# Performance work log

Hardware: AMD Instinct MI355X
Metric: run time of the kernel (lower is better)

Reference implementation:

```python
import jax, jax.numpy as jnp
import numpy as np
import math

B, T, C, H, E = 1, 384, 512, 8, 16
D = C // H

def layer_norm(x, w, b, eps=1e-5):
    mu = jnp.mean(x, axis=-1, keepdims=True)
    var = jnp.mean(jnp.square(x - mu), axis=-1, keepdims=True)
    return (x - mu) * jax.lax.rsqrt(var + eps) * w + b

def setup_inputs() -> dict:
    key = jax.random.key(0)
    ks = jax.random.split(key, 12)
    s = 0.02
    return {
        'x': jax.random.normal(ks[0], (B, T, C), jnp.float32),
        'bias_matrix': jax.random.randint(ks[1], (B, T, T), 0, E, jnp.int32),
        'ln1_w': jnp.ones((C,), jnp.float32),
        'ln1_b': jnp.zeros((C,), jnp.float32),
        'w_attn_w': jax.random.normal(ks[2], (3 * C, C), jnp.float32) * s,
        'w_attn_b': jnp.zeros((3 * C,), jnp.float32),
        'w_proj_w': jax.random.normal(ks[3], (C, C), jnp.float32) * s,
        'w_proj_b': jnp.zeros((C,), jnp.float32),
        'attn_bias_emb': jax.random.normal(ks[4], (E, H), jnp.float32) * s,
        'edge_emb': jax.random.normal(ks[5], (E, C), jnp.float32) * s,
        'w_edge_k_w': jax.random.normal(ks[6], (C, C), jnp.float32) * s,
        'w_edge_k_b': jnp.zeros((C,), jnp.float32),
        'w_edge_v_w': jax.random.normal(ks[7], (C, C), jnp.float32) * s,
        'w_edge_v_b': jnp.zeros((C,), jnp.float32),
        'ln2_w': jnp.ones((C,), jnp.float32),
        'ln2_b': jnp.zeros((C,), jnp.float32),
        'c_fc_w': jax.random.normal(ks[8], (4 * C, C), jnp.float32) * s,
        'c_fc_b': jnp.zeros((4 * C,), jnp.float32),
        'c_proj_w': jax.random.normal(ks[9], (C, 4 * C), jnp.float32) * s,
        'c_proj_b': jnp.zeros((C,), jnp.float32),
    }

def reference(x, bias_matrix, ln1_w, ln1_b, w_attn_w, w_attn_b, w_proj_w, w_proj_b,
              attn_bias_emb, edge_emb, w_edge_k_w, w_edge_k_b, w_edge_v_w, w_edge_v_b,
              ln2_w, ln2_b, c_fc_w, c_fc_b, c_proj_w, c_proj_b):
    # --- attention branch ---
    h = layer_norm(x, ln1_w, ln1_b)
    qkv = h @ w_attn_w.T + w_attn_b                      # (B,T,3C)
    q, k, v = jnp.split(qkv, 3, axis=-1)
    q = q.reshape(B, T, H, D).transpose(0, 2, 1, 3)      # (B,H,T,D)
    k = k.reshape(B, T, H, D).transpose(0, 2, 1, 3)
    v = v.reshape(B, T, H, D).transpose(0, 2, 1, 3)
    scale = math.sqrt(D)

    ee = edge_emb[bias_matrix]                           # (B,T,T,C)
    e_k = (ee @ w_edge_k_w.T + w_edge_k_b).reshape(B, T, T, H, D)
    # score[b,h,i,j] = sum_d q[b,h,i,d] * k[b,h,j,d] * e_k[b,i,j,h,d]
    scores = jnp.einsum('bhid,bhjd,bijhd->bhij', q, k, e_k) / scale

    mask = jnp.tril(jnp.ones((T, T), bool))              # causal, diag included
    scores = jnp.where(mask, scores, -jnp.inf)
    ab = attn_bias_emb[bias_matrix].transpose(0, 3, 1, 2)  # (B,H,T,T)
    ab = jnp.where(mask, ab, 0.0)
    attn = jax.nn.softmax(scores + ab, axis=-1)

    e_v = (ee @ w_edge_v_w.T + w_edge_v_b).reshape(B, T, T, H, D)
    # y[b,h,i,d] = sum_j attn[b,h,i,j] * v[b,h,j,d] * e_v[b,i,j,h,d]
    y = jnp.einsum('bhij,bhjd,bijhd->bhid', attn, v, e_v)
    y = y.transpose(0, 2, 1, 3).reshape(B, T, C)
    y = y @ w_proj_w.T + w_proj_b
    x = x + y

    # --- MLP branch ---
    h2 = layer_norm(x, ln2_w, ln2_b)
    h2 = jax.nn.gelu(h2 @ c_fc_w.T + c_fc_b, approximate=False)
    x = x + (h2 @ c_proj_w.T + c_proj_b)
    return x
```

## Files before the change

### kernel.cpp

```cpp
#include <hip/hip_runtime.h>
#include <math.h>

#define TT 384
#define CC 512
#define HH 8
#define EE 16

typedef __bf16 bf16_t;
typedef __bf16 bf16x8 __attribute__((ext_vector_type(8)));
typedef __bf16 bf16x4v __attribute__((ext_vector_type(4)));
typedef float f32x4 __attribute__((ext_vector_type(4)));

__device__ __forceinline__ float wave_reduce_sum(float v) {
#pragma unroll
  for (int off = 32; off >= 1; off >>= 1) v += __shfl_xor(v, off, 64);
  return v;
}
__device__ __forceinline__ float wave_reduce_max(float v) {
#pragma unroll
  for (int off = 32; off >= 1; off >>= 1) v = fmaxf(v, __shfl_xor(v, off, 64));
  return v;
}

struct PreArgs {
  const float *x, *ln1w, *ln1b, *wattn, *wattnb, *eemb, *wekw, *wekb, *wevw,
      *wevb, *ln2w, *ln2b, *cfcw, *cfcb, *wproj, *wcproj;
  float *ektab, *evtab, *xmu, *xrs, *x1s1, *x1s2, *s1q, *cq, *s1f, *cf;
  bf16_t *wqkv_bf, *wfc_bf, *wproj_bf, *wcproj_bf;
};

__device__ __forceinline__ void wrow_unit(const float* __restrict__ wr,
                                          const float* __restrict__ g,
                                          const float* __restrict__ bb,
                                          float extra_c, bf16_t* __restrict__ orow,
                                          float* __restrict__ s1p,
                                          float* __restrict__ cp, int lane) {
  const float* p = wr + lane * 8;
  f32x4 w0 = *(const f32x4*)p, w1 = *(const f32x4*)(p + 4);
  f32x4 g0 = *(const f32x4*)(g + lane * 8), g1 = *(const f32x4*)(g + lane * 8 + 4);
  f32x4 b0 = *(const f32x4*)(bb + lane * 8), b1 = *(const f32x4*)(bb + lane * 8 + 4);
  f32x4 p0 = w0 * g0, p1 = w1 * g1;
  bf16x8 o;
  o[0] = (bf16_t)p0.x; o[1] = (bf16_t)p0.y; o[2] = (bf16_t)p0.z; o[3] = (bf16_t)p0.w;
  o[4] = (bf16_t)p1.x; o[5] = (bf16_t)p1.y; o[6] = (bf16_t)p1.z; o[7] = (bf16_t)p1.w;
  *(bf16x8*)(orow + lane * 8) = o;
  float s1 = p0.x + p0.y + p0.z + p0.w + p1.x + p1.y + p1.z + p1.w;
  float c = w0.x * b0.x + w0.y * b0.y + w0.z * b0.z + w0.w * b0.w +
            w1.x * b1.x + w1.y * b1.y + w1.z * b1.z + w1.w * b1.w;
  s1 = wave_reduce_sum(s1);
  c = wave_reduce_sum(c);
  if (lane == 0) { *s1p = s1; *cp = c + extra_c; }
}

__global__ __launch_bounds__(256) void pre_k(PreArgs P) {
  int b = blockIdx.x, tid = threadIdx.x, lane = tid & 63, wave = tid >> 6;
  if (b < 256) {
    int wid = b * 4 + wave;
    int gbase = wid * 16;
    int table = gbase >> 13;
    int e = (gbase >> 9) & 15;
    int c0 = gbase & 511;
    const float* er = P.eemb + e * 512 + lane * 8;
    f32x4 ea = *(const f32x4*)er;
    f32x4 eb = *(const f32x4*)(er + 4);
    const float* wbase = table ? P.wevw : P.wekw;
    const float* bbase = table ? P.wevb : P.wekb;
    float* obase = (table ? P.evtab : P.ektab) + e * 512;
#pragma unroll
    for (int o = 0; o < 16; o++) {
      int c = c0 + o;
      const float* wr = wbase + (size_t)c * 512 + lane * 8;
      f32x4 wa = *(const f32x4*)wr;
      f32x4 wb = *(const f32x4*)(wr + 4);
      float acc = ea.x * wa.x + ea.y * wa.y + ea.z * wa.z + ea.w * wa.w +
                  eb.x * wb.x + eb.y * wb.y + eb.z * wb.z + eb.w * wb.w;
      acc = wave_reduce_sum(acc);
      if (lane == 0) obase[c] = acc + bbase[c];
    }
  } else if (b < 640) {
    int n = (b - 256) * 4 + wave;
    wrow_unit(P.wattn + (size_t)n * 512, P.ln1w, P.ln1b, P.wattnb[n],
              P.wqkv_bf + (size_t)n * 512, P.s1q + n, P.cq + n, lane);
  } else if (b < 1152) {
    int n = (b - 640) * 4 + wave;
    wrow_unit(P.cfcw + (size_t)n * 512, P.ln2w, P.ln2b, P.cfcb[n],
              P.wfc_bf + (size_t)n * 512, P.s1f + n, P.cf + n, lane);
  } else if (b < 1216) {
    int base = (b - 1152) * 1024;
    for (int u = tid; u < 1024; u += 256) {
      f32x4 a = *((const f32x4*)P.wproj + base + u);
      bf16x4v o;
      o[0] = (bf16_t)a.x; o[1] = (bf16_t)a.y; o[2] = (bf16_t)a.z; o[3] = (bf16_t)a.w;
      *((bf16x4v*)P.wproj_bf + base + u) = o;
    }
  } else if (b < 1472) {
    int base = (b - 1216) * 1024;
    for (int u = tid; u < 1024; u += 256) {
      f32x4 a = *((const f32x4*)P.wcproj + base + u);
      bf16x4v o;
      o[0] = (bf16_t)a.x; o[1] = (bf16_t)a.y; o[2] = (bf16_t)a.z; o[3] = (bf16_t)a.w;
      *((bf16x4v*)P.wcproj_bf + base + u) = o;
    }
  } else if (b < 1568) {
    int r = (b - 1472) * 4 + wave;
    const float* xr = P.x + (size_t)r * 512 + lane * 8;
    f32x4 a = *(const f32x4*)xr, c = *(const f32x4*)(xr + 4);
    float s = a.x + a.y + a.z + a.w + c.x + c.y + c.z + c.w;
    float q = a.x * a.x + a.y * a.y + a.z * a.z + a.w * a.w +
              c.x * c.x + c.y * c.y + c.z * c.z + c.w * c.w;
    s = wave_reduce_sum(s);
    q = wave_reduce_sum(q);
    if (lane == 0) {
      float mu = s * (1.0f / 512.0f);
      float var = q * (1.0f / 512.0f) - mu * mu;
      P.xmu[r] = mu;
      P.xrs[r] = rsqrtf(var + 1e-5f);
    }
  } else {
    for (int i = tid; i < 384; i += 256) { P.x1s1[i] = 0.f; P.x1s2[i] = 0.f; }
  }
}

template <int MODE>
__global__ __launch_bounds__(256) void gemm_k(
    const void* __restrict__ Aptr, const bf16_t* __restrict__ Wb,
    const float* __restrict__ e0, const float* __restrict__ e1,
    const float* __restrict__ e2, const float* __restrict__ e3,
    const float* __restrict__ res, void* __restrict__ out,
    float* __restrict__ st1, float* __restrict__ st2, int N, int K) {
  constexpr bool AF32 = (MODE == 0 || MODE == 2);
  __shared__ float part[4][32][32];
  int tid = threadIdx.x, lane = tid & 63, wave = tid >> 6;
  int m0 = blockIdx.y * 32, n0 = blockIdx.x * 32;
  int r16 = lane & 15, quad = lane >> 4;
  int kchunk = K >> 2, k0 = wave * kchunk;

  f32x4 acc[2][2];
  f32x4 zero = {0.f, 0.f, 0.f, 0.f};
#pragma unroll
  for (int i = 0; i < 2; i++)
#pragma unroll
    for (int j = 0; j < 2; j++) acc[i][j] = zero;

  const float* Af = (const float*)Aptr + (size_t)(m0 + r16) * K + k0 + quad * 8;
  const bf16_t* Ab = (const bf16_t*)Aptr + (size_t)(m0 + r16) * K + k0 + quad * 8;
  const bf16_t* Wp = Wb + (size_t)(n0 + r16) * K + k0 + quad * 8;
  for (int kb = 0; kb < kchunk; kb += 32) {
    bf16x8 af[2], bfr[2];
#pragma unroll
    for (int t = 0; t < 2; t++) {
      if (AF32) {
        f32x4 a = *(const f32x4*)(Af + (size_t)t * 16 * K + kb);
        f32x4 c = *(const f32x4*)(Af + (size_t)t * 16 * K + kb + 4);
        af[t][0] = (bf16_t)a.x; af[t][1] = (bf16_t)a.y;
        af[t][2] = (bf16_t)a.z; af[t][3] = (bf16_t)a.w;
        af[t][4] = (bf16_t)c.x; af[t][5] = (bf16_t)c.y;
        af[t][6] = (bf16_t)c.z; af[t][7] = (bf16_t)c.w;
      } else {
        af[t] = *(const bf16x8*)(Ab + (size_t)t * 16 * K + kb);
      }
    }
#pragma unroll
    for (int t = 0; t < 2; t++)
      bfr[t] = *(const bf16x8*)(Wp + (size_t)t * 16 * K + kb);
#pragma unroll
    for (int i = 0; i < 2; i++)
#pragma unroll
      for (int j = 0; j < 2; j++)
        acc[i][j] = __builtin_amdgcn_mfma_f32_16x16x32_bf16(af[i], bfr[j],
                                                            acc[i][j], 0, 0, 0);
  }

#pragma unroll
  for (int i = 0; i < 2; i++)
#pragma unroll
    for (int j = 0; j < 2; j++)
#pragma unroll
      for (int r = 0; r < 4; r++)
        part[wave][i * 16 + quad * 4 + r][j * 16 + r16] = acc[i][j][r];
  __syncthreads();

  int row = tid >> 3, c4 = (tid & 7) * 4;
  f32x4 v = *(const f32x4*)&part[0][row][c4];
  v += *(const f32x4*)&part[1][row][c4];
  v += *(const f32x4*)&part[2][row][c4];
  v += *(const f32x4*)&part[3][row][c4];
  int grow = m0 + row, gcol = n0 + c4;

  if (MODE == 0 || MODE == 2) {
    float mu, rs;
    if (MODE == 0) {
      mu = e0[grow]; rs = e1[grow];
    } else {
      float S = e0[grow], Q = e1[grow];
      mu = S * (1.0f / 512.0f);
      float var = Q * (1.0f / 512.0f) - mu * mu;
      rs = rsqrtf(var + 1e-5f);
    }
    f32x4 s1v = *(const f32x4*)(e2 + gcol);
    f32x4 ccv = *(const f32x4*)(e3 + gcol);
#pragma unroll
    for (int t = 0; t < 4; t++) {
      float x = rs * (v[t] - mu * s1v[t]) + ccv[t];
      if (MODE == 2) x = 0.5f * x * (1.0f + erff(x * 0.70710678118654752f));
      v[t] = x;
    }
    bf16x4v o;
#pragma unroll
    for (int t = 0; t < 4; t++) o[t] = (bf16_t)v[t];
    *(bf16x4v*)((bf16_t*)out + (size_t)grow * N + gcol) = o;
  } else {
    v += *(const f32x4*)(e2 + gcol);
    v += *(const f32x4*)(res + (size_t)grow * N + gcol);
    *(f32x4*)((float*)out + (size_t)grow * N + gcol) = v;
    if (MODE == 1) {
      float sv = v.x + v.y + v.z + v.w;
      float qv = v.x * v.x + v.y * v.y + v.z * v.z + v.w * v.w;
      sv += __shfl_down(sv, 4, 8); qv += __shfl_down(qv, 4, 8);
      sv += __shfl_down(sv, 2, 8); qv += __shfl_down(qv, 2, 8);
      sv += __shfl_down(sv, 1, 8); qv += __shfl_down(qv, 1, 8);
      if ((tid & 7) == 0) {
        atomicAdd(st1 + grow, sv);
        atomicAdd(st2 + grow, qv);
      }
    }
  }
}

__global__ __launch_bounds__(256) void attn_k(
    const bf16_t* __restrict__ qkv, const int* __restrict__ bias_matrix,
    const float* __restrict__ attn_bias_emb, const float* __restrict__ ek_tab,
    const float* __restrict__ ev_tab, bf16_t* __restrict__ ybuf) {
  __shared__ float s[TT];
  __shared__ int ebuf[TT];
  __shared__ float qe[EE][68];
  __shared__ float evh[EE * 64];
  __shared__ float red[4 * 64];
  __shared__ float absh[EE];
  __shared__ float scr[8];

  int i = blockIdx.x, h = blockIdx.y;
  int tid = threadIdx.x, lane = tid & 63, wave = tid >> 6;
  int n = i + 1;

  for (int j = tid; j < n; j += 256) ebuf[j] = bias_matrix[i * TT + j];
  if (tid < EE) absh[tid] = attn_bias_emb[tid * HH + h];
  for (int idx = tid; idx < EE * 64; idx += 256) {
    int e = idx >> 6, d = idx & 63;
    float qv = (float)qkv[(size_t)i * 1536 + h * 64 + d];
    qe[e][d] = qv * ek_tab[e * 512 + h * 64 + d];
    evh[idx] = ev_tab[e * 512 + h * 64 + d];
  }
  __syncthreads();

  for (int jl = tid; jl < n; jl += 256) {
    int e = ebuf[jl];
    const uint4* kp = (const uint4*)(qkv + (size_t)jl * 1536 + 512 + h * 64);
    uint4 kr[8];
#pragma unroll
    for (int dg = 0; dg < 8; dg++) kr[dg] = kp[dg];
    float acc = 0.f;
#pragma unroll
    for (int dg = 0; dg < 8; dg++) {
      bf16x8 kv = *reinterpret_cast<const bf16x8*>(&kr[dg]);
      f32x4 qa = *(const f32x4*)&qe[e][dg * 8];
      f32x4 qb = *(const f32x4*)&qe[e][dg * 8 + 4];
      acc += (float)kv[0] * qa.x + (float)kv[1] * qa.y + (float)kv[2] * qa.z +
             (float)kv[3] * qa.w + (float)kv[4] * qb.x + (float)kv[5] * qb.y +
             (float)kv[6] * qb.z + (float)kv[7] * qb.w;
    }
    s[jl] = acc * 0.125f + absh[e];
  }
  __syncthreads();

  float lm = -1e30f;
  for (int j = tid; j < n; j += 256) lm = fmaxf(lm, s[j]);
  lm = wave_reduce_max(lm);
  if (lane == 0) scr[wave] = lm;
  __syncthreads();
  float mx = fmaxf(fmaxf(scr[0], scr[1]), fmaxf(scr[2], scr[3]));
  float ls = 0.0f;
  for (int j = tid; j < n; j += 256) {
    float p = __expf(s[j] - mx);
    s[j] = p;
    ls += p;
  }
  ls = wave_reduce_sum(ls);
  if (lane == 0) scr[4 + wave] = ls;
  __syncthreads();
  float inv = 1.0f / (scr[4] + scr[5] + scr[6] + scr[7]);

  float acc = 0.0f;
  int j = wave;
  for (; j + 4 < n; j += 8) {
    int e0 = ebuf[j], e1 = ebuf[j + 4];
    float p0 = s[j], p1 = s[j + 4];
    float v0 = (float)qkv[(size_t)j * 1536 + 1024 + h * 64 + lane];
    float v1 = (float)qkv[(size_t)(j + 4) * 1536 + 1024 + h * 64 + lane];
    acc += p0 * v0 * evh[e0 * 64 + lane] + p1 * v1 * evh[e1 * 64 + lane];
  }
  for (; j < n; j += 4) {
    int e = ebuf[j];
    float vv = (float)qkv[(size_t)j * 1536 + 1024 + h * 64 + lane];
    acc += s[j] * vv * evh[e * 64 + lane];
  }
  red[wave * 64 + lane] = acc;
  __syncthreads();
  if (tid < 64) {
    float y = (red[tid] + red[64 + tid] + red[128 + tid] + red[192 + tid]) * inv;
    ybuf[(size_t)i * CC + h * 64 + tid] = (bf16_t)y;
  }
}

extern "C" void kernel_launch(void* const* d_in, const int* in_sizes, int n_in,
                              void* d_out, int out_size, void* d_ws,
                              size_t ws_size, hipStream_t stream) {
  const float* x = (const float*)d_in[0];
  const int* bias_mat = (const int*)d_in[1];

  char* wp = (char*)d_ws;
  float* ektab = (float*)wp;  wp += 16 * 512 * 4;
  float* evtab = (float*)wp;  wp += 16 * 512 * 4;
  float* xmu = (float*)wp;    wp += 384 * 4;
  float* xrs = (float*)wp;    wp += 384 * 4;
  float* x1s1 = (float*)wp;   wp += 384 * 4;
  float* x1s2 = (float*)wp;   wp += 384 * 4;
  float* s1q = (float*)wp;    wp += 1536 * 4;
  float* cq = (float*)wp;     wp += 1536 * 4;
  float* s1f = (float*)wp;    wp += 2048 * 4;
  float* cf = (float*)wp;     wp += 2048 * 4;
  float* x1 = (float*)wp;     wp += 384 * 512 * 4;
  bf16_t* wqkv_bf = (bf16_t*)wp;   wp += 1536 * 512 * 2;
  bf16_t* wfc_bf = (bf16_t*)wp;    wp += 2048 * 512 * 2;
  bf16_t* wproj_bf = (bf16_t*)wp;  wp += 512 * 512 * 2;
  bf16_t* wcproj_bf = (bf16_t*)wp; wp += 512 * 2048 * 2;
  bf16_t* qkv = (bf16_t*)wp;  wp += 384 * 1536 * 2;
  bf16_t* ybuf = (bf16_t*)wp; wp += 384 * 512 * 2;
  bf16_t* gbuf = (bf16_t*)wp; wp += 384 * 2048 * 2;

  PreArgs P;
  P.x = x;
  P.ln1w = (const float*)d_in[2];
  P.ln1b = (const float*)d_in[3];
  P.wattn = (const float*)d_in[4];
  P.wattnb = (const float*)d_in[5];
  P.eemb = (const float*)d_in[9];
  P.wekw = (const float*)d_in[10];
  P.wekb = (const float*)d_in[11];
  P.wevw = (const float*)d_in[12];
  P.wevb = (const float*)d_in[13];
  P.ln2w = (const float*)d_in[14];
  P.ln2b = (const float*)d_in[15];
  P.cfcw = (const float*)d_in[16];
  P.cfcb = (const float*)d_in[17];
  P.wproj = (const float*)d_in[6];
  P.wcproj = (const float*)d_in[18];
  P.ektab = ektab; P.evtab = evtab; P.xmu = xmu; P.xrs = xrs;
  P.x1s1 = x1s1; P.x1s2 = x1s2; P.s1q = s1q; P.cq = cq; P.s1f = s1f; P.cf = cf;
  P.wqkv_bf = wqkv_bf; P.wfc_bf = wfc_bf; P.wproj_bf = wproj_bf;
  P.wcproj_bf = wcproj_bf;

  pre_k<<<1569, 256, 0, stream>>>(P);
  gemm_k<0><<<dim3(48, 12), 256, 0, stream>>>(x, wqkv_bf, xmu, xrs, s1q, cq,
                                              nullptr, qkv, nullptr, nullptr,
                                              1536, 512);
  attn_k<<<dim3(TT, HH), 256, 0, stream>>>(qkv, bias_mat,
                                           (const float*)d_in[8], ektab, evtab,
                                           ybuf);
  gemm_k<1><<<dim3(16, 12), 256, 0, stream>>>(
      ybuf, wproj_bf, nullptr, nullptr, (const float*)d_in[7], nullptr, x, x1,
      x1s1, x1s2, 512, 512);
  gemm_k<2><<<dim3(64, 12), 256, 0, stream>>>(x1, wfc_bf, x1s1, x1s2, s1f, cf,
                                              nullptr, gbuf, nullptr, nullptr,
                                              2048, 512);
  gemm_k<3><<<dim3(16, 12), 256, 0, stream>>>(
      gbuf, wcproj_bf, nullptr, nullptr, (const float*)d_in[19], nullptr, x1,
      d_out, nullptr, nullptr, 512, 2048);
}
```

Baseline: 177.0 us.

## Batch four query rows per attention block and move weight prep into later kernels

The attention kernel now handles four consecutive query rows per block. Each loaded K/V row is reused across those four rows, blocks are ordered largest-first to balance the causal workload, and the bias indices are stored as bytes. Conversion of the c_fc, c_proj and w_proj weights moves out of the preprocessing kernel into extra grid rows of the QKV GEMM and attention kernels, where it runs alongside the main work. This is meant to cut redundant K/V traffic and shorten the serial preprocessing stage. In exchange it raises shared memory per block and adds branch divergence in the masked accumulation loops.

```diff
diff --git a/kernel.cpp b/kernel.cpp
--- a/kernel.cpp
+++ b/kernel.cpp
@@ -21,13 +21,6 @@
   for (int off = 32; off >= 1; off >>= 1) v = fmaxf(v, __shfl_xor(v, off, 64));
   return v;
 }
-
-struct PreArgs {
-  const float *x, *ln1w, *ln1b, *wattn, *wattnb, *eemb, *wekw, *wekb, *wevw,
-      *wevb, *ln2w, *ln2b, *cfcw, *cfcb, *wproj, *wcproj;
-  float *ektab, *evtab, *xmu, *xrs, *x1s1, *x1s2, *s1q, *cq, *s1f, *cf;
-  bf16_t *wqkv_bf, *wfc_bf, *wproj_bf, *wcproj_bf;
-};
 
 __device__ __forceinline__ void wrow_unit(const float* __restrict__ wr,
                                           const float* __restrict__ g,
@@ -52,6 +45,13 @@
   if (lane == 0) { *s1p = s1; *cp = c + extra_c; }
 }
 
+struct PreArgs {
+  const float *x, *ln1w, *ln1b, *wattn, *wattnb, *eemb, *wekw, *wekb, *wevw,
+      *wevb;
+  float *ektab, *evtab, *xmu, *xrs, *x1s1, *x1s2, *s1q, *cq;
+  bf16_t* wqkv_bf;
+};
+
 __global__ __launch_bounds__(256) void pre_k(PreArgs P) {
   int b = blockIdx.x, tid = threadIdx.x, lane = tid & 63, wave = tid >> 6;
   if (b < 256) {
@@ -81,28 +81,8 @@
     int n = (b - 256) * 4 + wave;
     wrow_unit(P.wattn + (size_t)n * 512, P.ln1w, P.ln1b, P.wattnb[n],
               P.wqkv_bf + (size_t)n * 512, P.s1q + n, P.cq + n, lane);
-  } else if (b < 1152) {
-    int n = (b - 640) * 4 + wave;
-    wrow_unit(P.cfcw + (size_t)n * 512, P.ln2w, P.ln2b, P.cfcb[n],
-              P.wfc_bf + (size_t)n * 512, P.s1f + n, P.cf + n, lane);
-  } else if (b < 1216) {
-    int base = (b - 1152) * 1024;
-    for (int u = tid; u < 1024; u += 256) {
-      f32x4 a = *((const f32x4*)P.wproj + base + u);
-      bf16x4v o;
-      o[0] = (bf16_t)a.x; o[1] = (bf16_t)a.y; o[2] = (bf16_t)a.z; o[3] = (bf16_t)a.w;
-      *((bf16x4v*)P.wproj_bf + base + u) = o;
-    }
-  } else if (b < 1472) {
-    int base = (b - 1216) * 1024;
-    for (int u = tid; u < 1024; u += 256) {
-      f32x4 a = *((const f32x4*)P.wcproj + base + u);
-      bf16x4v o;
-      o[0] = (bf16_t)a.x; o[1] = (bf16_t)a.y; o[2] = (bf16_t)a.z; o[3] = (bf16_t)a.w;
-      *((bf16x4v*)P.wcproj_bf + base + u) = o;
-    }
-  } else if (b < 1568) {
-    int r = (b - 1472) * 4 + wave;
+  } else if (b < 736) {
+    int r = (b - 640) * 4 + wave;
     const float* xr = P.x + (size_t)r * 512 + lane * 8;
     f32x4 a = *(const f32x4*)xr, c = *(const f32x4*)(xr + 4);
     float s = a.x + a.y + a.z + a.w + c.x + c.y + c.z + c.w;
@@ -127,10 +107,22 @@
     const float* __restrict__ e0, const float* __restrict__ e1,
     const float* __restrict__ e2, const float* __restrict__ e3,
     const float* __restrict__ res, void* __restrict__ out,
-    float* __restrict__ st1, float* __restrict__ st2, int N, int K) {
+    float* __restrict__ st1, float* __restrict__ st2, int N, int K,
+    const float* __restrict__ cw, bf16_t* __restrict__ cwb, int cwn) {
   constexpr bool AF32 = (MODE == 0 || MODE == 2);
+  int tid = threadIdx.x;
+  if (MODE == 0 && blockIdx.y == 12) {
+    int stride = gridDim.x * 256;
+    for (int u = blockIdx.x * 256 + tid; u < cwn; u += stride) {
+      f32x4 a = *((const f32x4*)cw + u);
+      bf16x4v o;
+      o[0] = (bf16_t)a.x; o[1] = (bf16_t)a.y; o[2] = (bf16_t)a.z; o[3] = (bf16_t)a.w;
+      *((bf16x4v*)cwb + u) = o;
+    }
+    return;
+  }
   __shared__ float part[4][32][32];
-  int tid = threadIdx.x, lane = tid & 63, wave = tid >> 6;
+  int lane = tid & 63, wave = tid >> 6;
   int m0 = blockIdx.y * 32, n0 = blockIdx.x * 32;
   int r16 = lane & 15, quad = lane >> 4;
   int kchunk = K >> 2, k0 = wave * kchunk;
@@ -228,87 +220,132 @@
 }
 
 __global__ __launch_bounds__(256) void attn_k(
-    const bf16_t* __restrict__ qkv, const int* __restrict__ bias_matrix,
-    const float* __restrict__ attn_bias_emb, const float* __restrict__ ek_tab,
-    const float* __restrict__ ev_tab, bf16_t* __restrict__ ybuf) {
-  __shared__ float s[TT];
-  __shared__ int ebuf[TT];
-  __shared__ float qe[EE][68];
-  __shared__ float evh[EE * 64];
-  __shared__ float red[4 * 64];
+    const bf16_t* __restrict__ qkv, const int* __restrict__ bm,
+    const float* __restrict__ abemb, const float* __restrict__ ektab,
+    const float* __restrict__ evtab, bf16_t* __restrict__ ybuf,
+    const float* __restrict__ ln2w, const float* __restrict__ ln2b,
+    const float* __restrict__ cfcw, const float* __restrict__ cfcb,
+    bf16_t* __restrict__ wfc_bf, float* __restrict__ s1f,
+    float* __restrict__ cf, const float* __restrict__ wcproj,
+    bf16_t* __restrict__ wcproj_bf) {
+  int tid = threadIdx.x, lane = tid & 63, wave = tid >> 6;
+  int by = blockIdx.y, bx = blockIdx.x;
+
+  if (by == 8) {
+    for (int n = bx * 4 + wave; n < 2048; n += 384)
+      wrow_unit(cfcw + (size_t)n * 512, ln2w, ln2b, cfcb[n],
+                wfc_bf + (size_t)n * 512, s1f + n, cf + n, lane);
+    return;
+  }
+  if (by == 9) {
+    for (int u = bx * 256 + tid; u < 262144; u += 96 * 256) {
+      f32x4 a = *((const f32x4*)wcproj + u);
+      bf16x4v o;
+      o[0] = (bf16_t)a.x; o[1] = (bf16_t)a.y; o[2] = (bf16_t)a.z; o[3] = (bf16_t)a.w;
+      *((bf16x4v*)wcproj_bf + u) = o;
+    }
+    return;
+  }
+
+  __shared__ float s[4][TT];
+  __shared__ unsigned char eb[4][TT];
+  __shared__ float qe[4][EE][68];
+  __shared__ float evh[EE][64];
+  __shared__ float red[4][4][64];
   __shared__ float absh[EE];
-  __shared__ float scr[8];
-
-  int i = blockIdx.x, h = blockIdx.y;
-  int tid = threadIdx.x, lane = tid & 63, wave = tid >> 6;
-  int n = i + 1;
-
-  for (int j = tid; j < n; j += 256) ebuf[j] = bias_matrix[i * TT + j];
-  if (tid < EE) absh[tid] = attn_bias_emb[tid * HH + h];
-  for (int idx = tid; idx < EE * 64; idx += 256) {
-    int e = idx >> 6, d = idx & 63;
-    float qv = (float)qkv[(size_t)i * 1536 + h * 64 + d];
-    qe[e][d] = qv * ek_tab[e * 512 + h * 64 + d];
-    evh[idx] = ev_tab[e * 512 + h * 64 + d];
-  }
+  __shared__ float inv4[4];
+
+  int h = by;
+  int g = 95 - bx;
+  int i0 = g * 4;
+  int nmax = i0 + 4;
+
+  for (int idx = tid; idx < 4 * TT; idx += 256) {
+    int i2 = idx / TT, j = idx % TT;
+    eb[i2][j] = (unsigned char)bm[(i0 + i2) * TT + j];
+  }
+  if (tid < EE) absh[tid] = abemb[tid * HH + h];
+  for (int idx = tid; idx < 4 * EE * 64; idx += 256) {
+    int i2 = idx >> 10, r = idx & 1023, e = r >> 6, d = r & 63;
+    float qv = (float)qkv[(size_t)(i0 + i2) * 1536 + h * 64 + d];
+    qe[i2][e][d] = qv * ektab[e * 512 + h * 64 + d];
+  }
+  for (int idx = tid; idx < EE * 64; idx += 256)
+    evh[idx >> 6][idx & 63] = evtab[(idx >> 6) * 512 + h * 64 + (idx & 63)];
   __syncthreads();
 
-  for (int jl = tid; jl < n; jl += 256) {
-    int e = ebuf[jl];
+  for (int jl = tid; jl < nmax; jl += 256) {
     const uint4* kp = (const uint4*)(qkv + (size_t)jl * 1536 + 512 + h * 64);
     uint4 kr[8];
 #pragma unroll
     for (int dg = 0; dg < 8; dg++) kr[dg] = kp[dg];
-    float acc = 0.f;
+    int e_[4];
+#pragma unroll
+    for (int i2 = 0; i2 < 4; i2++) e_[i2] = eb[i2][jl];
+    float ac[4] = {0.f, 0.f, 0.f, 0.f};
 #pragma unroll
     for (int dg = 0; dg < 8; dg++) {
       bf16x8 kv = *reinterpret_cast<const bf16x8*>(&kr[dg]);
-      f32x4 qa = *(const f32x4*)&qe[e][dg * 8];
-      f32x4 qb = *(const f32x4*)&qe[e][dg * 8 + 4];
-      acc += (float)kv[0] * qa.x + (float)kv[1] * qa.y + (float)kv[2] * qa.z +
-             (float)kv[3] * qa.w + (float)kv[4] * qb.x + (float)kv[5] * qb.y +
-             (float)kv[6] * qb.z + (float)kv[7] * qb.w;
-    }
-    s[jl] = acc * 0.125f + absh[e];
+      float kf[8];
+#pragma unroll
+      for (int t = 0; t < 8; t++) kf[t] = (float)kv[t];
+#pragma unroll
+      for (int i2 = 0; i2 < 4; i2++) {
+        const float* qp = &qe[i2][e_[i2]][dg * 8];
+        f32x4 qa = *(const f32x4*)qp;
+        f32x4 qb = *(const f32x4*)(qp + 4);
+        ac[i2] += kf[0] * qa.x + kf[1] * qa.y + kf[2] * qa.z + kf[3] * qa.w +
+                  kf[4] * qb.x + kf[5] * qb.y + kf[6] * qb.z + kf[7] * qb.w;
+      }
+    }
+#pragma unroll
+    for (int i2 = 0; i2 < 4; i2++)
+      if (jl <= i0 + i2) s[i2][jl] = ac[i2] * 0.125f + absh[e_[i2]];
   }
   __syncthreads();
 
-  float lm = -1e30f;
-  for (int j = tid; j < n; j += 256) lm = fmaxf(lm, s[j]);
-  lm = wave_reduce_max(lm);
-  if (lane == 0) scr[wave] = lm;
+  {
+    int i2 = wave, n = i0 + i2 + 1;
+    float lm = -1e30f;
+    for (int j = lane; j < n; j += 64) lm = fmaxf(lm, s[i2][j]);
+    lm = wave_reduce_max(lm);
+    float ls = 0.f;
+    for (int j = lane; j < n; j += 64) {
+      float p = __expf(s[i2][j] - lm);
+      s[i2][j] = p;
+      ls += p;
+    }
+    ls = wave_reduce_sum(ls);
+    if (lane == 0) inv4[i2] = 1.0f / ls;
+  }
   __syncthreads();
-  float mx = fmaxf(fmaxf(scr[0], scr[1]), fmaxf(scr[2], scr[3]));
-  float ls = 0.0f;
-  for (int j = tid; j < n; j += 256) {
-    float p = __expf(s[j] - mx);
-    s[j] = p;
-    ls += p;
-  }
-  ls = wave_reduce_sum(ls);
-  if (lane == 0) scr[4 + wave] = ls;
+
+  float acc[4] = {0.f, 0.f, 0.f, 0.f};
+  int j = wave;
+  for (; j + 4 < nmax; j += 8) {
+    float va = (float)qkv[(size_t)j * 1536 + 1024 + h * 64 + lane];
+    float vb = (float)qkv[(size_t)(j + 4) * 1536 + 1024 + h * 64 + lane];
+#pragma unroll
+    for (int i2 = 0; i2 < 4; i2++) {
+      if (j <= i0 + i2) acc[i2] += s[i2][j] * va * evh[eb[i2][j]][lane];
+      if (j + 4 <= i0 + i2)
+        acc[i2] += s[i2][j + 4] * vb * evh[eb[i2][j + 4]][lane];
+    }
+  }
+  for (; j < nmax; j += 4) {
+    float va = (float)qkv[(size_t)j * 1536 + 1024 + h * 64 + lane];
+#pragma unroll
+    for (int i2 = 0; i2 < 4; i2++)
+      if (j <= i0 + i2) acc[i2] += s[i2][j] * va * evh[eb[i2][j]][lane];
+  }
+#pragma unroll
+  for (int i2 = 0; i2 < 4; i2++) red[wave][i2][lane] = acc[i2];
   __syncthreads();
-  float inv = 1.0f / (scr[4] + scr[5] + scr[6] + scr[7]);
-
-  float acc = 0.0f;
-  int j = wave;
-  for (; j + 4 < n; j += 8) {
-    int e0 = ebuf[j], e1 = ebuf[j + 4];
-    float p0 = s[j], p1 = s[j + 4];
-    float v0 = (float)qkv[(size_t)j * 1536 + 1024 + h * 64 + lane];
-    float v1 = (float)qkv[(size_t)(j + 4) * 1536 + 1024 + h * 64 + lane];
-    acc += p0 * v0 * evh[e0 * 64 + lane] + p1 * v1 * evh[e1 * 64 + lane];
-  }
-  for (; j < n; j += 4) {
-    int e = ebuf[j];
-    float vv = (float)qkv[(size_t)j * 1536 + 1024 + h * 64 + lane];
-    acc += s[j] * vv * evh[e * 64 + lane];
-  }
-  red[wave * 64 + lane] = acc;
-  __syncthreads();
-  if (tid < 64) {
-    float y = (red[tid] + red[64 + tid] + red[128 + tid] + red[192 + tid]) * inv;
-    ybuf[(size_t)i * CC + h * 64 + tid] = (bf16_t)y;
+  {
+    int i2 = tid >> 6, d = tid & 63;
+    float y = (red[0][i2][d] + red[1][i2][d] + red[2][i2][d] + red[3][i2][d]) *
+              inv4[i2];
+    ybuf[(size_t)(i0 + i2) * CC + h * 64 + d] = (bf16_t)y;
   }
 }
 
@@ -349,31 +386,26 @@
   P.wekb = (const float*)d_in[11];
   P.wevw = (const float*)d_in[12];
   P.wevb = (const float*)d_in[13];
-  P.ln2w = (const float*)d_in[14];
-  P.ln2b = (const float*)d_in[15];
-  P.cfcw = (const float*)d_in[16];
-  P.cfcb = (const float*)d_in[17];
-  P.wproj = (const float*)d_in[6];
-  P.wcproj = (const float*)d_in[18];
   P.ektab = ektab; P.evtab = evtab; P.xmu = xmu; P.xrs = xrs;
-  P.x1s1 = x1s1; P.x1s2 = x1s2; P.s1q = s1q; P.cq = cq; P.s1f = s1f; P.cf = cf;
-  P.wqkv_bf = wqkv_bf; P.wfc_bf = wfc_bf; P.wproj_bf = wproj_bf;
-  P.wcproj_bf = wcproj_bf;
-
-  pre_k<<<1569, 256, 0, stream>>>(P);
-  gemm_k<0><<<dim3(48, 12), 256, 0, stream>>>(x, wqkv_bf, xmu, xrs, s1q, cq,
-                                              nullptr, qkv, nullptr, nullptr,
-                                              1536, 512);
-  attn_k<<<dim3(TT, HH), 256, 0, stream>>>(qkv, bias_mat,
-                                           (const float*)d_in[8], ektab, evtab,
-                                           ybuf);
+  P.x1s1 = x1s1; P.x1s2 = x1s2; P.s1q = s1q; P.cq = cq;
+  P.wqkv_bf = wqkv_bf;
+
+  pre_k<<<737, 256, 0, stream>>>(P);
+  gemm_k<0><<<dim3(48, 13), 256, 0, stream>>>(
+      x, wqkv_bf, xmu, xrs, s1q, cq, nullptr, qkv, nullptr, nullptr, 1536, 512,
+      (const float*)d_in[6], wproj_bf, 65536);
+  attn_k<<<dim3(96, 10), 256, 0, stream>>>(
+      qkv, bias_mat, (const float*)d_in[8], ektab, evtab, ybuf,
+      (const float*)d_in[14], (const float*)d_in[15], (const float*)d_in[16],
+      (const float*)d_in[17], wfc_bf, s1f, cf, (const float*)d_in[18],
+      wcproj_bf);
   gemm_k<1><<<dim3(16, 12), 256, 0, stream>>>(
       ybuf, wproj_bf, nullptr, nullptr, (const float*)d_in[7], nullptr, x, x1,
-      x1s1, x1s2, 512, 512);
-  gemm_k<2><<<dim3(64, 12), 256, 0, stream>>>(x1, wfc_bf, x1s1, x1s2, s1f, cf,
-                                              nullptr, gbuf, nullptr, nullptr,
-                                              2048, 512);
+      x1s1, x1s2, 512, 512, nullptr, nullptr, 0);
+  gemm_k<2><<<dim3(64, 12), 256, 0, stream>>>(
+      x1, wfc_bf, x1s1, x1s2, s1f, cf, nullptr, gbuf, nullptr, nullptr, 2048,
+      512, nullptr, nullptr, 0);
   gemm_k<3><<<dim3(16, 12), 256, 0, stream>>>(
       gbuf, wcproj_bf, nullptr, nullptr, (const float*)d_in[19], nullptr, x1,
-      d_out, nullptr, nullptr, 512, 2048);
-}
+      d_out, nullptr, nullptr, 512, 2048, nullptr, nullptr, 0);
+}
```

Result: slower. 260.7 us (+47.3%).
